# Optimization experiments

Measured on AMD Instinct MI355X. Metric: run time of the kernel, lower is better.

Reference implementation:

```python
import jax, jax.numpy as jnp
import numpy as np

N_EMBD = 1024
N_HEAD = 16
HEAD_SIZE = N_EMBD // N_HEAD
SEQ_LEN = 2048


def setup_inputs() -> dict:
    key = jax.random.key(0)
    k_x, k_wa, k_ba, k_wp, k_bp = jax.random.split(key, 5)
    s = 0.02
    return {
        "x": jax.random.normal(k_x, (4, SEQ_LEN, N_EMBD), dtype=jnp.float32),
        "w_attn": jax.random.normal(k_wa, (N_EMBD, 3 * N_EMBD), dtype=jnp.float32) * s,
        "b_attn": jax.random.normal(k_ba, (3 * N_EMBD,), dtype=jnp.float32) * s,
        "w_proj": jax.random.normal(k_wp, (N_EMBD, N_EMBD), dtype=jnp.float32) * s,
        "b_proj": jax.random.normal(k_bp, (N_EMBD,), dtype=jnp.float32) * s,
    }


def reference(x, w_attn, b_attn, w_proj, b_proj):
    B, T, C = x.shape
    H, D = N_HEAD, HEAD_SIZE
    qkv = x @ w_attn + b_attn                      # [B,T,3C]
    q, k, v = jnp.split(qkv, 3, axis=-1)
    q = q.reshape(B, T, H, D).transpose(0, 2, 1, 3)  # [B,H,T,D]
    k = k.reshape(B, T, H, D).transpose(0, 2, 1, 3)
    v = v.reshape(B, T, H, D).transpose(0, 2, 1, 3)
    att = jnp.einsum('bhqd,bhkd->bhqk', q, k) / jnp.sqrt(jnp.float32(D))
    causal = jnp.tril(jnp.ones((T, T), dtype=bool))
    att = jnp.where(causal[None, None], att, jnp.float32(-jnp.inf))
    att = jax.nn.softmax(att, axis=-1)
    out = jnp.einsum('bhqk,bhkd->bhqd', att, v)    # [B,H,T,D]
    out = out.transpose(0, 2, 1, 3).reshape(B, T, C)
    return out @ w_proj + b_proj
```

## Files before the change

kernel.cpp:

```cpp
#include <hip/hip_runtime.h>

typedef short short8 __attribute__((ext_vector_type(8)));
typedef short short4v __attribute__((ext_vector_type(4)));
typedef float f32x4 __attribute__((ext_vector_type(4)));
typedef unsigned uint2v __attribute__((ext_vector_type(2)));

__device__ __forceinline__ float bf2f(short b) {
  unsigned u = ((unsigned)(unsigned short)b) << 16;
  return __builtin_bit_cast(float, u);
}
__device__ __forceinline__ short f2bf(float f) {
  unsigned u = __builtin_bit_cast(unsigned, f);
  u += 0x7fffu + ((u >> 16) & 1u);
  return (short)(u >> 16);
}
__device__ __forceinline__ unsigned cvt_pk_bf16(float lo, float hi) {
  unsigned r;
  asm("v_cvt_pk_bf16_f32 %0, %1, %2" : "=v"(r) : "v"(lo), "v"(hi));
  return r;
}

__device__ __forceinline__ void gload_lds16(const void* g, void* l) {
  __builtin_amdgcn_global_load_lds(
      (const __attribute__((address_space(1))) unsigned int*)g,
      (__attribute__((address_space(3))) unsigned int*)l, 16, 0, 0);
}

__device__ __forceinline__ short8 lds_frag(const short* tile, int row, int kc, int l4) {
  int chunk = (kc * 4 + l4) ^ (row & 7);
  return *(const short8*)&tile[row * 64 + chunk * 8];
}

__global__ __launch_bounds__(256) void k_convert_bf16(const float* __restrict__ in,
                                                      short* __restrict__ out, int n8) {
  int i = blockIdx.x * 256 + threadIdx.x;
  if (i >= n8) return;
  const float4* p = (const float4*)in;
  float4 a = p[2 * i], b = p[2 * i + 1];
  short8 o;
  o[0] = f2bf(a.x); o[1] = f2bf(a.y); o[2] = f2bf(a.z); o[3] = f2bf(a.w);
  o[4] = f2bf(b.x); o[5] = f2bf(b.y); o[6] = f2bf(b.z); o[7] = f2bf(b.w);
  ((short8*)out)[i] = o;
}

__global__ __launch_bounds__(256) void k_transpose_w(const float* __restrict__ w,
                                                     short* __restrict__ wT, int K, int N) {
  __shared__ float t[32][33];
  int nt = N >> 5;
  int rt = blockIdx.x / nt, ct = blockIdx.x % nt;
  int tx = threadIdx.x & 31, ty = threadIdx.x >> 5;
#pragma unroll
  for (int i = 0; i < 4; ++i) {
    int r = ty * 4 + i;
    t[r][tx] = w[(size_t)(rt * 32 + r) * N + ct * 32 + tx];
  }
  __syncthreads();
#pragma unroll
  for (int i = 0; i < 4; ++i) {
    int r = ty * 4 + i;
    wT[(size_t)(ct * 32 + r) * K + rt * 32 + tx] = f2bf(t[tx][r]);
  }
}

template <bool BF16OUT>
__global__ __launch_bounds__(512, 1) void k_gemm8p(const short* __restrict__ A,
                                                   const short* __restrict__ Bt,
                                                   const float* __restrict__ bias,
                                                   void* __restrict__ Cout,
                                                   short* __restrict__ vTout,
                                                   int M, int N, int K) {
  __shared__ __align__(16) short Ab[2][256 * 64];
  __shared__ __align__(16) short Bb[2][256 * 64];
  int nt = N >> 8;
  int nwg = gridDim.x;
  int bid = blockIdx.x;
  int swz = (bid & 7) * (nwg >> 3) + (bid >> 3);
  int mt = swz / nt, ct = swz % nt;
  int tid = threadIdx.x, w = tid >> 6, lane = tid & 63;
  int l15 = lane & 15, l4 = lane >> 4;
  int wm = w >> 2, wn = w & 3;
  const short* Abase = A + (size_t)mt * 256 * K;
  const short* Bbase = Bt + (size_t)ct * 256 * K;
  int NT = K >> 6;

  int srow = lane >> 3;
  int slc = (lane & 7) ^ srow;

  auto stage = [&](const short* gbase, short* dstTile, int kt, int half) {
#pragma unroll
    for (int i = 0; i < 2; ++i) {
      int rowg = half * 128 + i * 64 + w * 8;
      gload_lds16(gbase + (size_t)(rowg + srow) * K + kt * 64 + slc * 8,
                  dstTile + (size_t)rowg * 64);
    }
  };

  f32x4 acc[8][4];
#pragma unroll
  for (int m = 0; m < 8; ++m)
#pragma unroll
    for (int n = 0; n < 4; ++n) acc[m][n] = f32x4{0.f, 0.f, 0.f, 0.f};

  stage(Bbase, &Bb[0][0], 0, 0);
  stage(Bbase, &Bb[0][0], 0, 1);
  stage(Abase, &Ab[0][0], 0, 0);
  stage(Abase, &Ab[0][0], 0, 1);
  stage(Bbase, &Bb[1][0], 1, 0);
  stage(Bbase, &Bb[1][0], 1, 1);
  stage(Abase, &Ab[1][0], 1, 0);
  stage(Abase, &Ab[1][0], 1, 1);
  asm volatile("s_waitcnt vmcnt(8)" ::: "memory");
  __builtin_amdgcn_s_barrier();

  for (int t = 0; t < NT; ++t) {
    int b = t & 1;
    const short* At = &Ab[b][0];
    const short* Btl = &Bb[b][0];
    short* Aw = &Ab[b][0];
    short* Bw = &Bb[b][0];
    bool pre = (t + 2 < NT);

    short8 aflo[4][2], bflo[2][2], bfhi[2][2], afhi[4][2];
#pragma unroll
    for (int mq = 0; mq < 4; ++mq)
#pragma unroll
      for (int kc = 0; kc < 2; ++kc)
        aflo[mq][kc] = lds_frag(At, wm * 128 + mq * 16 + l15, kc, l4);
#pragma unroll
    for (int nq = 0; nq < 2; ++nq)
#pragma unroll
      for (int kc = 0; kc < 2; ++kc)
        bflo[nq][kc] = lds_frag(Btl, wn * 64 + nq * 16 + l15, kc, l4);
    __builtin_amdgcn_s_barrier();
    asm volatile("s_waitcnt lgkmcnt(0)" ::: "memory");
    __builtin_amdgcn_sched_barrier(0);
    __builtin_amdgcn_s_setprio(1);
#pragma unroll
    for (int mq = 0; mq < 4; ++mq)
#pragma unroll
      for (int nq = 0; nq < 2; ++nq)
#pragma unroll
        for (int kc = 0; kc < 2; ++kc)
          acc[mq][nq] = __builtin_amdgcn_mfma_f32_16x16x32_bf16(aflo[mq][kc], bflo[nq][kc], acc[mq][nq], 0, 0, 0);
    __builtin_amdgcn_s_setprio(0);
    __builtin_amdgcn_s_barrier();

#pragma unroll
    for (int nq = 0; nq < 2; ++nq)
#pragma unroll
      for (int kc = 0; kc < 2; ++kc)
        bfhi[nq][kc] = lds_frag(Btl, wn * 64 + 32 + nq * 16 + l15, kc, l4);
    __builtin_amdgcn_s_barrier();
    asm volatile("s_waitcnt lgkmcnt(0)" ::: "memory");
    __builtin_amdgcn_sched_barrier(0);
    __builtin_amdgcn_s_setprio(1);
#pragma unroll
    for (int mq = 0; mq < 4; ++mq)
#pragma unroll
      for (int nq = 0; nq < 2; ++nq)
#pragma unroll
        for (int kc = 0; kc < 2; ++kc)
          acc[mq][2 + nq] = __builtin_amdgcn_mfma_f32_16x16x32_bf16(aflo[mq][kc], bfhi[nq][kc], acc[mq][2 + nq], 0, 0, 0);
    __builtin_amdgcn_s_setprio(0);
    __builtin_amdgcn_s_barrier();

#pragma unroll
    for (int mq = 0; mq < 4; ++mq)
#pragma unroll
      for (int kc = 0; kc < 2; ++kc)
        afhi[mq][kc] = lds_frag(At, wm * 128 + 64 + mq * 16 + l15, kc, l4);
    if (pre) {
      stage(Bbase, Bw, t + 2, 0);
      stage(Bbase, Bw, t + 2, 1);
    }
    __builtin_amdgcn_s_barrier();
    asm volatile("s_waitcnt lgkmcnt(0)" ::: "memory");
    __builtin_amdgcn_sched_barrier(0);
    __builtin_amdgcn_s_setprio(1);
#pragma unroll
    for (int mq = 0; mq < 4; ++mq)
#pragma unroll
      for (int nq = 0; nq < 2; ++nq)
#pragma unroll
        for (int kc = 0; kc < 2; ++kc)
          acc[4 + mq][2 + nq] = __builtin_amdgcn_mfma_f32_16x16x32_bf16(afhi[mq][kc], bfhi[nq][kc], acc[4 + mq][2 + nq], 0, 0, 0);
    __builtin_amdgcn_s_setprio(0);
    __builtin_amdgcn_s_barrier();

    if (pre) {
      stage(Abase, Aw, t + 2, 0);
      stage(Abase, Aw, t + 2, 1);
    }
    __builtin_amdgcn_s_setprio(1);
#pragma unroll
    for (int mq = 0; mq < 4; ++mq)
#pragma unroll
      for (int nq = 0; nq < 2; ++nq)
#pragma unroll
        for (int kc = 0; kc < 2; ++kc)
          acc[4 + mq][nq] = __builtin_amdgcn_mfma_f32_16x16x32_bf16(afhi[mq][kc], bflo[nq][kc], acc[4 + mq][nq], 0, 0, 0);
    __builtin_amdgcn_s_setprio(0);
    if (pre) {
      asm volatile("s_waitcnt vmcnt(8)" ::: "memory");
    } else if (t + 1 < NT) {
      asm volatile("s_waitcnt vmcnt(0)" ::: "memory");
    }
    __builtin_amdgcn_s_barrier();
  }

#pragma unroll
  for (int m = 0; m < 8; ++m) {
#pragma unroll
    for (int n = 0; n < 4; ++n) {
      int row = mt * 256 + wm * 128 + m * 16 + l4 * 4;
      int col = ct * 256 + wn * 64 + n * 16 + l15;
      float bv = bias[col];
      if constexpr (BF16OUT) {
        short4v pk4;
#pragma unroll
        for (int j = 0; j < 4; ++j) pk4[j] = f2bf(acc[m][n][j] + bv);
        if (col >= 2048) {
          int hh = (col - 2048) >> 6, dd = (col - 2048) & 63;
          int batch2 = row >> 11, tok = row & 2047;
          *(short4v*)(vTout + (((size_t)(batch2 * 16 + hh) * 64 + dd) << 11) + tok) = pk4;
        } else {
#pragma unroll
          for (int j = 0; j < 4; ++j)
            ((short*)Cout)[(size_t)(row + j) * N + col] = pk4[j];
        }
      } else {
#pragma unroll
        for (int j = 0; j < 4; ++j)
          ((float*)Cout)[(size_t)(row + j) * N + col] = acc[m][n][j] + bv;
      }
    }
  }
}

template <bool BF16OUT>
__global__ __launch_bounds__(256) void k_gemm_bt(const short* __restrict__ A,
                                                 const short* __restrict__ Bt,
                                                 const float* __restrict__ bias,
                                                 void* __restrict__ Cout,
                                                 int M, int N, int K) {
  __shared__ __align__(16) short As[128 * 32];
  __shared__ __align__(16) short Bs[128 * 32];
  int nt = N >> 7;
  int mt = blockIdx.x / nt, ct = blockIdx.x % nt;
  int tid = threadIdx.x, w = tid >> 6, lane = tid & 63;
  int l15 = lane & 15, l4 = lane >> 4;
  int wr = (w >> 1) * 64, wc = (w & 1) * 64;
  const short* Abase = A + (size_t)mt * 128 * K;
  const short* Bbase = Bt + (size_t)ct * 128 * K;
  f32x4 acc[4][4];
#pragma unroll
  for (int m = 0; m < 4; ++m)
#pragma unroll
    for (int n = 0; n < 4; ++n) acc[m][n] = f32x4{0.f, 0.f, 0.f, 0.f};

  for (int kt = 0; kt < K; kt += 32) {
    __syncthreads();
#pragma unroll
    for (int i = 0; i < 2; ++i) {
      int idx = (w * 2 + i) * 64 + lane;
      gload_lds16(Abase + (size_t)(idx >> 2) * K + kt + (idx & 3) * 8, &As[(w * 2 + i) * 512]);
      gload_lds16(Bbase + (size_t)(idx >> 2) * K + kt + (idx & 3) * 8, &Bs[(w * 2 + i) * 512]);
    }
    __syncthreads();
    short8 af[4], bfr[4];
#pragma unroll
    for (int m = 0; m < 4; ++m) af[m] = *(const short8*)&As[(wr + m * 16 + l15) * 32 + l4 * 8];
#pragma unroll
    for (int n = 0; n < 4; ++n) bfr[n] = *(const short8*)&Bs[(wc + n * 16 + l15) * 32 + l4 * 8];
#pragma unroll
    for (int m = 0; m < 4; ++m)
#pragma unroll
      for (int n = 0; n < 4; ++n)
        acc[m][n] = __builtin_amdgcn_mfma_f32_16x16x32_bf16(af[m], bfr[n], acc[m][n], 0, 0, 0);
  }

#pragma unroll
  for (int m = 0; m < 4; ++m) {
#pragma unroll
    for (int n = 0; n < 4; ++n) {
      int row = mt * 128 + wr + m * 16 + l4 * 4;
      int col = ct * 128 + wc + n * 16 + l15;
      float bv = bias[col];
#pragma unroll
      for (int j = 0; j < 4; ++j) {
        float v = acc[m][n][j] + bv;
        if constexpr (BF16OUT)
          ((short*)Cout)[(size_t)(row + j) * N + col] = f2bf(v);
        else
          ((float*)Cout)[(size_t)(row + j) * N + col] = v;
      }
    }
  }
}

__global__ __launch_bounds__(256, 2) void k_attn(const short* __restrict__ qkv,
                                                 const short* __restrict__ vT,
                                                 short* __restrict__ out) {
  constexpr int T = 2048, C3 = 3072;
  __shared__ __align__(16) short Kl[2][64 * 72];
  __shared__ __align__(16) short P_lds[4][32 * 72];
  int i_ = blockIdx.x;
  int xcd = i_ & 7, m_ = i_ >> 3;
  int bh = xcd * 8 + (m_ & 7), bp = m_ >> 3;
  int batch = bh >> 4, h = bh & 15;
  int tid = threadIdx.x, w = tid >> 6, lane = tid & 63;
  int l15 = lane & 15, l4 = lane >> 4;

  int qt[2];
  qt[0] = 63 - (bp * 4 + w);
  qt[1] = bp * 4 + w;
  int lim[2] = {qt[0] >> 1, qt[1] >> 1};
  int ktb = (63 - bp * 4) >> 1;

  const short* kbase = qkv + (size_t)(batch * T) * C3 + 1024 + h * 64;
  const short* vbase = vT + (size_t)bh * 64 * T;

  int sr0 = tid >> 3, sr1 = 32 + (tid >> 3), sdc = (tid & 7) * 8;

  const float SCL = 0.18033688f;
  short8 qf[2][2][2];
#pragma unroll
  for (int t = 0; t < 2; ++t)
#pragma unroll
    for (int qc = 0; qc < 2; ++qc) {
      const short* qrow = qkv + (size_t)(batch * T + qt[t] * 32 + qc * 16 + l15) * C3 + h * 64;
#pragma unroll
      for (int kc = 0; kc < 2; ++kc) {
        short8 v = *(const short8*)(qrow + kc * 32 + l4 * 8);
#pragma unroll
        for (int i = 0; i < 8; ++i) v[i] = f2bf(bf2f(v[i]) * SCL);
        qf[t][qc][kc] = v;
      }
    }

  const f32x4 ZERO = f32x4{0.f, 0.f, 0.f, 0.f};
  short8 ONES;
#pragma unroll
  for (int i = 0; i < 8; ++i) ONES[i] = (short)0x3F80;

  f32x4 o_[2][2][4];
  f32x4 lacc[2][2];
#pragma unroll
  for (int t = 0; t < 2; ++t)
#pragma unroll
    for (int qc = 0; qc < 2; ++qc) {
      lacc[t][qc] = ZERO;
#pragma unroll
      for (int dt = 0; dt < 4; ++dt) o_[t][qc][dt] = ZERO;
    }

  {
    short8 a = *(const short8*)(kbase + (size_t)sr0 * C3 + sdc);
    short8 b = *(const short8*)(kbase + (size_t)sr1 * C3 + sdc);
    *(short8*)&Kl[0][sr0 * 72 + sdc] = a;
    *(short8*)&Kl[0][sr1 * 72 + sdc] = b;
  }
  __syncthreads();

  int cur = 0;
  for (int kt = 0; kt <= ktb; ++kt) {
    bool more = (kt < ktb);
    bool act0 = (kt <= lim[0]), act1 = (kt <= lim[1]);

    short8 pre0, pre1;
    if (more) {
      pre0 = *(const short8*)(kbase + (size_t)((kt + 1) * 64 + sr0) * C3 + sdc);
      pre1 = *(const short8*)(kbase + (size_t)((kt + 1) * 64 + sr1) * C3 + sdc);
    }

    const short* Kb = &Kl[cur][0];
    short8 kf[4][2];
#pragma unroll
    for (int kvt = 0; kvt < 4; ++kvt)
#pragma unroll
      for (int kc = 0; kc < 2; ++kc)
        kf[kvt][kc] = *(const short8*)(Kb + (kvt * 16 + l15) * 72 + kc * 32 + l4 * 8);

    short8 vf[4][2];
#pragma unroll
    for (int dt = 0; dt < 4; ++dt)
#pragma unroll
      for (int kc = 0; kc < 2; ++kc)
        vf[dt][kc] = *(const short8*)(vbase + (size_t)(dt * 16 + l15) * T + kt * 64 + kc * 32 + l4 * 8);

#pragma unroll
    for (int t = 0; t < 2; ++t) {
      bool act = (t == 0) ? act0 : act1;
      if (!act) continue;
      short* pb = &P_lds[w][0];

#pragma unroll
      for (int qc = 0; qc < 2; ++qc) {
        f32x4 s[4];
        __builtin_amdgcn_s_setprio(1);
#pragma unroll
        for (int kvt = 0; kvt < 4; ++kvt) {
          s[kvt] = __builtin_amdgcn_mfma_f32_16x16x32_bf16(kf[kvt][0], qf[t][qc][0], ZERO, 0, 0, 0);
          s[kvt] = __builtin_amdgcn_mfma_f32_16x16x32_bf16(kf[kvt][1], qf[t][qc][1], s[kvt], 0, 0, 0);
        }
        __builtin_amdgcn_s_setprio(0);

        if (kt == lim[t]) {
          int qg = qt[t] * 32 + qc * 16 + l15;
#pragma unroll
          for (int kvt = 0; kvt < 4; ++kvt)
#pragma unroll
            for (int j = 0; j < 4; ++j) {
              int kg = kt * 64 + kvt * 16 + l4 * 4 + j;
              if (kg > qg) s[kvt][j] = -1e30f;
            }
        }

#pragma unroll
        for (int kvt = 0; kvt < 4; ++kvt) {
          float p0 = exp2f(s[kvt][0]);
          float p1 = exp2f(s[kvt][1]);
          float p2 = exp2f(s[kvt][2]);
          float p3 = exp2f(s[kvt][3]);
          unsigned lo = cvt_pk_bf16(p0, p1);
          unsigned hi = cvt_pk_bf16(p2, p3);
          *(uint2v*)(pb + (qc * 16 + l15) * 72 + kvt * 16 + l4 * 4) = uint2v{lo, hi};
        }
      }

      asm volatile("s_waitcnt lgkmcnt(0)" ::: "memory");

      __builtin_amdgcn_s_setprio(1);
#pragma unroll
      for (int qc = 0; qc < 2; ++qc)
#pragma unroll
        for (int kc = 0; kc < 2; ++kc) {
          short8 pf = *(const short8*)(pb + (qc * 16 + l15) * 72 + kc * 32 + l4 * 8);
          lacc[t][qc] = __builtin_amdgcn_mfma_f32_16x16x32_bf16(ONES, pf, lacc[t][qc], 0, 0, 0);
#pragma unroll
          for (int dt = 0; dt < 4; ++dt)
            o_[t][qc][dt] = __builtin_amdgcn_mfma_f32_16x16x32_bf16(vf[dt][kc], pf, o_[t][qc][dt], 0, 0, 0);
        }
      __builtin_amdgcn_s_setprio(0);
    }

    if (more) {
      *(short8*)&Kl[cur ^ 1][sr0 * 72 + sdc] = pre0;
      *(short8*)&Kl[cur ^ 1][sr1 * 72 + sdc] = pre1;
    }
    __syncthreads();
    cur ^= 1;
  }

#pragma unroll
  for (int t = 0; t < 2; ++t) {
#pragma unroll
    for (int qc = 0; qc < 2; ++qc) {
      float inv = 1.f / lacc[t][qc][0];
      size_t rowb = (size_t)(batch * T + qt[t] * 32 + qc * 16 + l15) * 1024 + h * 64;
#pragma unroll
      for (int dt = 0; dt < 4; ++dt) {
        short4v pk4;
#pragma unroll
        for (int j = 0; j < 4; ++j) pk4[j] = f2bf(o_[t][qc][dt][j] * inv);
        *(short4v*)(out + rowb + dt * 16 + l4 * 4) = pk4;
      }
    }
  }
}

extern "C" void kernel_launch(void* const* d_in, const int* in_sizes, int n_in,
                              void* d_out, int out_size, void* d_ws, size_t ws_size,
                              hipStream_t stream) {
  const float* x      = (const float*)d_in[0];
  const float* w_attn = (const float*)d_in[1];
  const float* b_attn = (const float*)d_in[2];
  const float* w_proj = (const float*)d_in[3];
  const float* b_proj = (const float*)d_in[4];
  float* out = (float*)d_out;

  char* ws = (char*)d_ws;
  short* xb   = (short*)(ws);
  short* waT  = (short*)(ws + 16777216);
  short* wpT  = (short*)(ws + 23068672);
  short* qkv  = (short*)(ws + 25165824);
  short* vT   = (short*)(ws + 75497472);
  short* attn = xb;

  k_convert_bf16<<<4096, 256, 0, stream>>>(x, xb, 1048576);
  k_transpose_w<<<32 * 96, 256, 0, stream>>>(w_attn, waT, 1024, 3072);
  k_transpose_w<<<32 * 32, 256, 0, stream>>>(w_proj, wpT, 1024, 1024);
  k_gemm8p<true><<<384, 512, 0, stream>>>(xb, waT, b_attn, qkv, vT, 8192, 3072, 1024);
  k_attn<<<512, 256, 0, stream>>>(qkv, vT, attn);
  k_gemm_bt<false><<<64 * 8, 256, 0, stream>>>(attn, wpT, b_proj, out, 8192, 1024, 1024);
}
```

Measured before the change: 198.4 us.

## Split paired causal attention q-tiles into separate blocks, longest-first ordering

Each attention block used to handle two paired q-tiles (one long, one short) per wave so causal work was balanced within a block. Now each block handles a single group of four q-tiles, the grid doubles to 1024 blocks, blocks are issued with the heaviest groups first, and launch bounds ask for three blocks per CU. The goal is more parallelism and lower register pressure, relying on the scheduler to balance causal load instead of pairing. The trade-offs are that K tiles are loaded once per block, so global K traffic and the tile-loop overhead grow, and waves within a block now finish at uneven times.

```diff
diff --git a/kernel.cpp b/kernel.cpp
--- a/kernel.cpp
+++ b/kernel.cpp
@@ -298,7 +298,7 @@
   }
 }
 
-__global__ __launch_bounds__(256, 2) void k_attn(const short* __restrict__ qkv,
+__global__ __launch_bounds__(256, 3) void k_attn(const short* __restrict__ qkv,
                                                  const short* __restrict__ vT,
                                                  short* __restrict__ out) {
   constexpr int T = 2048, C3 = 3072;
@@ -306,16 +306,15 @@
   __shared__ __align__(16) short P_lds[4][32 * 72];
   int i_ = blockIdx.x;
   int xcd = i_ & 7, m_ = i_ >> 3;
-  int bh = xcd * 8 + (m_ & 7), bp = m_ >> 3;
+  int bh = xcd * 8 + (m_ & 7);
+  int g = 15 - (m_ >> 3);
   int batch = bh >> 4, h = bh & 15;
   int tid = threadIdx.x, w = tid >> 6, lane = tid & 63;
   int l15 = lane & 15, l4 = lane >> 4;
 
-  int qt[2];
-  qt[0] = 63 - (bp * 4 + w);
-  qt[1] = bp * 4 + w;
-  int lim[2] = {qt[0] >> 1, qt[1] >> 1};
-  int ktb = (63 - bp * 4) >> 1;
+  int qt = 4 * g + w;
+  int lim = qt >> 1;
+  int ktb = (4 * g + 3) >> 1;
 
   const short* kbase = qkv + (size_t)(batch * T) * C3 + 1024 + h * 64;
   const short* vbase = vT + (size_t)bh * 64 * T;
@@ -323,36 +322,32 @@
   int sr0 = tid >> 3, sr1 = 32 + (tid >> 3), sdc = (tid & 7) * 8;
 
   const float SCL = 0.18033688f;
-  short8 qf[2][2][2];
-#pragma unroll
-  for (int t = 0; t < 2; ++t)
-#pragma unroll
-    for (int qc = 0; qc < 2; ++qc) {
-      const short* qrow = qkv + (size_t)(batch * T + qt[t] * 32 + qc * 16 + l15) * C3 + h * 64;
-#pragma unroll
-      for (int kc = 0; kc < 2; ++kc) {
-        short8 v = *(const short8*)(qrow + kc * 32 + l4 * 8);
-#pragma unroll
-        for (int i = 0; i < 8; ++i) v[i] = f2bf(bf2f(v[i]) * SCL);
-        qf[t][qc][kc] = v;
-      }
-    }
+  short8 qf[2][2];
+#pragma unroll
+  for (int qc = 0; qc < 2; ++qc) {
+    const short* qrow = qkv + (size_t)(batch * T + qt * 32 + qc * 16 + l15) * C3 + h * 64;
+#pragma unroll
+    for (int kc = 0; kc < 2; ++kc) {
+      short8 v = *(const short8*)(qrow + kc * 32 + l4 * 8);
+#pragma unroll
+      for (int i = 0; i < 8; ++i) v[i] = f2bf(bf2f(v[i]) * SCL);
+      qf[qc][kc] = v;
+    }
+  }
 
   const f32x4 ZERO = f32x4{0.f, 0.f, 0.f, 0.f};
   short8 ONES;
 #pragma unroll
   for (int i = 0; i < 8; ++i) ONES[i] = (short)0x3F80;
 
-  f32x4 o_[2][2][4];
-  f32x4 lacc[2][2];
-#pragma unroll
-  for (int t = 0; t < 2; ++t)
-#pragma unroll
-    for (int qc = 0; qc < 2; ++qc) {
-      lacc[t][qc] = ZERO;
-#pragma unroll
-      for (int dt = 0; dt < 4; ++dt) o_[t][qc][dt] = ZERO;
-    }
+  f32x4 o_[2][4];
+  f32x4 lacc[2];
+#pragma unroll
+  for (int qc = 0; qc < 2; ++qc) {
+    lacc[qc] = ZERO;
+#pragma unroll
+    for (int dt = 0; dt < 4; ++dt) o_[qc][dt] = ZERO;
+  }
 
   {
     short8 a = *(const short8*)(kbase + (size_t)sr0 * C3 + sdc);
@@ -365,7 +360,7 @@
   int cur = 0;
   for (int kt = 0; kt <= ktb; ++kt) {
     bool more = (kt < ktb);
-    bool act0 = (kt <= lim[0]), act1 = (kt <= lim[1]);
+    bool act = (kt <= lim);
 
     short8 pre0, pre1;
     if (more) {
@@ -373,40 +368,36 @@
       pre1 = *(const short8*)(kbase + (size_t)((kt + 1) * 64 + sr1) * C3 + sdc);
     }
 
-    const short* Kb = &Kl[cur][0];
-    short8 kf[4][2];
-#pragma unroll
-    for (int kvt = 0; kvt < 4; ++kvt)
-#pragma unroll
-      for (int kc = 0; kc < 2; ++kc)
-        kf[kvt][kc] = *(const short8*)(Kb + (kvt * 16 + l15) * 72 + kc * 32 + l4 * 8);
-
-    short8 vf[4][2];
-#pragma unroll
-    for (int dt = 0; dt < 4; ++dt)
-#pragma unroll
-      for (int kc = 0; kc < 2; ++kc)
-        vf[dt][kc] = *(const short8*)(vbase + (size_t)(dt * 16 + l15) * T + kt * 64 + kc * 32 + l4 * 8);
-
-#pragma unroll
-    for (int t = 0; t < 2; ++t) {
-      bool act = (t == 0) ? act0 : act1;
-      if (!act) continue;
+    if (act) {
+      const short* Kb = &Kl[cur][0];
+      short8 kf[4][2];
+#pragma unroll
+      for (int kvt = 0; kvt < 4; ++kvt)
+#pragma unroll
+        for (int kc = 0; kc < 2; ++kc)
+          kf[kvt][kc] = *(const short8*)(Kb + (kvt * 16 + l15) * 72 + kc * 32 + l4 * 8);
+
+      short8 vf[4][2];
+#pragma unroll
+      for (int dt = 0; dt < 4; ++dt)
+#pragma unroll
+        for (int kc = 0; kc < 2; ++kc)
+          vf[dt][kc] = *(const short8*)(vbase + (size_t)(dt * 16 + l15) * T + kt * 64 + kc * 32 + l4 * 8);
+
       short* pb = &P_lds[w][0];
-
 #pragma unroll
       for (int qc = 0; qc < 2; ++qc) {
         f32x4 s[4];
         __builtin_amdgcn_s_setprio(1);
 #pragma unroll
         for (int kvt = 0; kvt < 4; ++kvt) {
-          s[kvt] = __builtin_amdgcn_mfma_f32_16x16x32_bf16(kf[kvt][0], qf[t][qc][0], ZERO, 0, 0, 0);
-          s[kvt] = __builtin_amdgcn_mfma_f32_16x16x32_bf16(kf[kvt][1], qf[t][qc][1], s[kvt], 0, 0, 0);
+          s[kvt] = __builtin_amdgcn_mfma_f32_16x16x32_bf16(kf[kvt][0], qf[qc][0], ZERO, 0, 0, 0);
+          s[kvt] = __builtin_amdgcn_mfma_f32_16x16x32_bf16(kf[kvt][1], qf[qc][1], s[kvt], 0, 0, 0);
         }
         __builtin_amdgcn_s_setprio(0);
 
-        if (kt == lim[t]) {
-          int qg = qt[t] * 32 + qc * 16 + l15;
+        if (kt == lim) {
+          int qg = qt * 32 + qc * 16 + l15;
 #pragma unroll
           for (int kvt = 0; kvt < 4; ++kvt)
 #pragma unroll
@@ -436,10 +427,10 @@
 #pragma unroll
         for (int kc = 0; kc < 2; ++kc) {
           short8 pf = *(const short8*)(pb + (qc * 16 + l15) * 72 + kc * 32 + l4 * 8);
-          lacc[t][qc] = __builtin_amdgcn_mfma_f32_16x16x32_bf16(ONES, pf, lacc[t][qc], 0, 0, 0);
+          lacc[qc] = __builtin_amdgcn_mfma_f32_16x16x32_bf16(ONES, pf, lacc[qc], 0, 0, 0);
 #pragma unroll
           for (int dt = 0; dt < 4; ++dt)
-            o_[t][qc][dt] = __builtin_amdgcn_mfma_f32_16x16x32_bf16(vf[dt][kc], pf, o_[t][qc][dt], 0, 0, 0);
+            o_[qc][dt] = __builtin_amdgcn_mfma_f32_16x16x32_bf16(vf[dt][kc], pf, o_[qc][dt], 0, 0, 0);
         }
       __builtin_amdgcn_s_setprio(0);
     }
@@ -453,18 +444,15 @@
   }
 
 #pragma unroll
-  for (int t = 0; t < 2; ++t) {
-#pragma unroll
-    for (int qc = 0; qc < 2; ++qc) {
-      float inv = 1.f / lacc[t][qc][0];
-      size_t rowb = (size_t)(batch * T + qt[t] * 32 + qc * 16 + l15) * 1024 + h * 64;
-#pragma unroll
-      for (int dt = 0; dt < 4; ++dt) {
-        short4v pk4;
-#pragma unroll
-        for (int j = 0; j < 4; ++j) pk4[j] = f2bf(o_[t][qc][dt][j] * inv);
-        *(short4v*)(out + rowb + dt * 16 + l4 * 4) = pk4;
-      }
+  for (int qc = 0; qc < 2; ++qc) {
+    float inv = 1.f / lacc[qc][0];
+    size_t rowb = (size_t)(batch * T + qt * 32 + qc * 16 + l15) * 1024 + h * 64;
+#pragma unroll
+    for (int dt = 0; dt < 4; ++dt) {
+      short4v pk4;
+#pragma unroll
+      for (int j = 0; j < 4; ++j) pk4[j] = f2bf(o_[qc][dt][j] * inv);
+      *(short4v*)(out + rowb + dt * 16 + l4 * 4) = pk4;
     }
   }
 }
@@ -491,6 +479,6 @@
   k_transpose_w<<<32 * 96, 256, 0, stream>>>(w_attn, waT, 1024, 3072);
   k_transpose_w<<<32 * 32, 256, 0, stream>>>(w_proj, wpT, 1024, 1024);
   k_gemm8p<true><<<384, 512, 0, stream>>>(xb, waT, b_attn, qkv, vT, 8192, 3072, 1024);
-  k_attn<<<512, 256, 0, stream>>>(qkv, vT, attn);
+  k_attn<<<1024, 256, 0, stream>>>(qkv, vT, attn);
   k_gemm_bt<false><<<64 * 8, 256, 0, stream>>>(attn, wpT, b_proj, out, 8192, 1024, 1024);
 }
```

Result: slower. 218.3 us (+10.1%).
